# Kernel optimization log

Hardware: AMD Instinct MI355X
Metric: run time of the kernel (lower is better)

Reference implementation:

```python
import jax, jax.numpy as jnp
import numpy as np

E, N, D, H = 600000, 100000, 128, 128
LN_EPS = 1e-5


def setup_inputs() -> dict:
    key = jax.random.key(0)
    ks = jax.random.split(key, 10)
    inp = {
        "efeat": jax.random.normal(ks[0], (E, D), dtype=jnp.float32),
        "nfeat": jax.random.normal(ks[1], (N, D), dtype=jnp.float32),
        "src_idx": jax.random.randint(ks[2], (E,), 0, N, dtype=jnp.int64) if jax.config.jax_enable_x64 else jax.random.randint(ks[2], (E,), 0, N, dtype=jnp.int32),
        "dst_idx": jax.random.randint(ks[3], (E,), 0, N, dtype=jnp.int32),
        # MLP params: Linear(3D -> H) + SiLU, Linear(H -> D), LayerNorm(D)
        "W1": jax.random.normal(ks[4], (3 * D, H), dtype=jnp.float32) / np.sqrt(3 * D),
        "b1": jnp.zeros((H,), dtype=jnp.float32),
        "W2": jax.random.normal(ks[5], (H, D), dtype=jnp.float32) / np.sqrt(H),
        "b2": jnp.zeros((D,), dtype=jnp.float32),
        "ln_scale": jnp.ones((D,), dtype=jnp.float32),
        "ln_bias": jnp.zeros((D,), dtype=jnp.float32),
    }
    return inp


def _layernorm(x, scale, bias):
    mu = jnp.mean(x, axis=-1, keepdims=True)
    var = jnp.mean(jnp.square(x - mu), axis=-1, keepdims=True)
    return (x - mu) * jax.lax.rsqrt(var + LN_EPS) * scale + bias


def reference(efeat, nfeat, src_idx, dst_idx, W1, b1, W2, b2, ln_scale, ln_bias):
    # Gather per-edge source/destination node features (irregular access).
    src = nfeat[src_idx]              # [E, D]
    dst = nfeat[dst_idx]              # [E, D]
    # TMLP: equivalent to concat([efeat, src, dst]) @ W1; expressed as split GEMMs
    # so no [E, 3D] concat buffer is materialized.
    Wf, Ws, Wd = W1[:D], W1[D:2 * D], W1[2 * D:]
    h = efeat @ Wf + src @ Ws + dst @ Wd + b1   # [E, H]
    h = jax.nn.silu(h)
    y = h @ W2 + b2                              # [E, D]
    y = _layernorm(y, ln_scale, ln_bias)
    efeat_new = y + efeat                        # residual add
    return (efeat_new, nfeat)
```

## Files before the change

### kernel.cpp

```cpp
#include <hip/hip_runtime.h>
#include <stdint.h>

#define E_N 600000
#define N_N 100000

typedef short short8   __attribute__((ext_vector_type(8)));
typedef short short8a  __attribute__((ext_vector_type(8), may_alias));
typedef float floatx4  __attribute__((ext_vector_type(4)));
typedef float floatx2  __attribute__((ext_vector_type(2)));
typedef float floatx4a __attribute__((ext_vector_type(4), may_alias));
typedef float floatx8a __attribute__((ext_vector_type(8), may_alias));
typedef unsigned int uintx2  __attribute__((ext_vector_type(2)));
typedef unsigned int uintx2a __attribute__((ext_vector_type(2), may_alias));
typedef unsigned int uintx4a __attribute__((ext_vector_type(4), may_alias));
typedef __bf16 bf16x4 __attribute__((ext_vector_type(4)));
typedef __bf16 bf16x8 __attribute__((ext_vector_type(8)));

static __device__ __forceinline__ unsigned short f2bf(float f){
  unsigned u = __builtin_bit_cast(unsigned, f);
  unsigned rnd = 0x7fffu + ((u >> 16) & 1u);
  return (unsigned short)((u + rnd) >> 16);
}
static __device__ __forceinline__ unsigned pk2(float a, float b){
  floatx2 f; f[0] = a; f[1] = b;
  typedef __bf16 bf16x2 __attribute__((ext_vector_type(2)));
  return __builtin_bit_cast(unsigned, __builtin_convertvector(f, bf16x2));
}

__global__ void prep_weights(const float* __restrict__ W1, const float* __restrict__ W2,
                             unsigned short* __restrict__ w1s, unsigned short* __restrict__ w2s){
  int i = blockIdx.x * 256 + threadIdx.x;
  if (i < 384 * 128){
    int c = i / 384, k = i - c * 384;
    int p = k >> 7, kp = k & 127;
    int dw = c * 64 + ((kp >> 1) ^ ((c & 7) << 2));
    w1s[p * 16384 + dw * 2 + (k & 1)] = f2bf(W1[k * 128 + c]);
  } else {
    int j = i - 384 * 128;
    int c = j >> 7, k = j & 127;
    int dw = c * 64 + ((k >> 1) ^ ((c & 7) << 2));
    w2s[dw * 2 + (k & 1)] = f2bf(W2[k * 128 + c]);
  }
}

__global__ void prep_nfeat(const float* __restrict__ nf,
                           unsigned* __restrict__ nfbu,
                           float* __restrict__ out2){
  const int total = N_N * 128 / 4;
  int stride = gridDim.x * blockDim.x;
  for (int i = blockIdx.x * blockDim.x + threadIdx.x; i < total; i += stride){
    float4 v = reinterpret_cast<const float4*>(nf)[i];
    reinterpret_cast<float4*>(out2)[i] = v;
    nfbu[2 * i]     = pk2(v.x, v.y);
    nfbu[2 * i + 1] = pk2(v.z, v.w);
  }
}

static __device__ __forceinline__ void glds16(void* lds, const void* g){
  __builtin_amdgcn_global_load_lds((const __attribute__((address_space(1))) unsigned int*)g,
                                   (__attribute__((address_space(3))) unsigned int*)lds,
                                   16, 0, 0);
}

__global__ __launch_bounds__(512, 4) void fused_edge(
    const float* __restrict__ efeat,
    const int* __restrict__ src_idx, const int* __restrict__ dst_idx,
    const unsigned short* __restrict__ nfb,
    const unsigned short* __restrict__ w1s, const unsigned short* __restrict__ w2s,
    const float* __restrict__ b1, const float* __restrict__ b2,
    const float* __restrict__ lns, const float* __restrict__ lnb,
    float* __restrict__ out)
{
  __shared__ __align__(16) unsigned char smem[67584];
  unsigned int* wlds  = (unsigned int*)smem;
  float*        cmisc = (float*)(smem + 65536);

  const int tid  = threadIdx.x;
  const int w    = tid >> 6;
  const int lane = tid & 63;
  const int r    = lane & 15;
  const int g    = lane >> 4;
  const int sw8  = (r & 7) << 2;

  unsigned int* tile = (unsigned int*)(smem + 32768 + w * 4096);

  auto stageW = [&](const unsigned short* src){
    #pragma unroll
    for (int rnd = 0; rnd < 4; ++rnd){
      int off = rnd * 8192 + tid * 16;
      glds16(smem + off, (const unsigned char*)src + off);
    }
  };

  stageW(w1s);
  cmisc[tid] = tid < 128 ? b1[tid] : tid < 256 ? b2[tid - 128]
             : tid < 384 ? lns[tid - 256] : lnb[tid - 384];

  const int eb = blockIdx.x * 128 + w * 16;

  int e0 = eb + r;
  const int er = e0 < E_N ? e0 : (E_N - 1);
  int si = src_idx[er];
  int di = dst_idx[er];
  si = si < 0 ? 0 : (si >= N_N ? N_N - 1 : si);
  di = di < 0 ? 0 : (di >= N_N ? N_N - 1 : di);

  auto loadX_f32 = [&](const float* p) -> short8 {
    floatx8a f = *reinterpret_cast<const floatx8a*>(p);
    return __builtin_bit_cast(short8, __builtin_convertvector(f, bf16x8));
  };

  short8 xf[12];
  #pragma unroll
  for (int kf = 0; kf < 4; ++kf)
    xf[kf] = loadX_f32(efeat + (size_t)er * 128 + kf * 32 + 8 * g);
  #pragma unroll
  for (int kf = 0; kf < 4; ++kf)
    xf[4 + kf] = *reinterpret_cast<const short8a*>(nfb + (size_t)si * 128 + kf * 32 + 8 * g);
  #pragma unroll
  for (int kf = 0; kf < 4; ++kf)
    xf[8 + kf] = *reinterpret_cast<const short8a*>(nfb + (size_t)di * 128 + kf * 32 + 8 * g);

  __syncthreads();

  auto loadWL = [&](int m, int k4) -> short8 {
    uintx4a v = *reinterpret_cast<const uintx4a*>(
        &wlds[(16 * m + r) * 64 + ((k4 * 16 + 4 * g) ^ sw8)]);
    return __builtin_bit_cast(short8, v);
  };

  floatx4 acc1[8];
  #pragma unroll
  for (int mi = 0; mi < 8; ++mi)
    acc1[mi] = (floatx4){0.f, 0.f, 0.f, 0.f};

  #pragma unroll
  for (int p = 0; p < 3; ++p){
    #pragma unroll
    for (int k4 = 0; k4 < 4; ++k4){
      short8 x = xf[p * 4 + k4];
      #pragma unroll
      for (int mi = 0; mi < 8; ++mi){
        short8 wf = loadWL(mi, k4);
        acc1[mi] = __builtin_amdgcn_mfma_f32_16x16x32_bf16(wf, x, acc1[mi], 0, 0, 0);
      }
    }
    if (p == 2){
      #pragma unroll
      for (int mi = 0; mi < 8; ++mi){
        floatx4 bb = *reinterpret_cast<const floatx4a*>(&cmisc[16 * mi + 4 * g]);
        floatx4 vv;
        #pragma unroll
        for (int q = 0; q < 4; ++q){
          float xx = acc1[mi][q] + bb[q];
          vv[q] = xx * __builtin_amdgcn_rcpf(1.f + __expf(-xx));
        }
        uintx2 pk = __builtin_bit_cast(uintx2, __builtin_convertvector(vv, bf16x4));
        *reinterpret_cast<uintx2a*>(&tile[r * 64 + ((8 * mi + 2 * g) ^ sw8)]) = pk;
      }
    }
    __syncthreads();
    if (p < 2) stageW(w1s + (p + 1) * 16384);
    else       stageW(w2s);
    __syncthreads();
  }

  floatx4 acc2[8];
  #pragma unroll
  for (int mo = 0; mo < 8; ++mo)
    acc2[mo] = (floatx4){0.f, 0.f, 0.f, 0.f};

  #pragma unroll
  for (int ks = 0; ks < 4; ++ks){
    uintx4a hv = *reinterpret_cast<const uintx4a*>(&tile[r * 64 + ((ks * 16 + 4 * g) ^ sw8)]);
    short8 hb = __builtin_bit_cast(short8, hv);
    #pragma unroll
    for (int mo = 0; mo < 8; ++mo){
      short8 wf = loadWL(mo, ks);
      acc2[mo] = __builtin_amdgcn_mfma_f32_16x16x32_bf16(wf, hb, acc2[mo], 0, 0, 0);
    }
  }

  const float* ef = efeat + (size_t)er * 128;
  floatx4 e4v[8];
  #pragma unroll
  for (int mo = 0; mo < 8; ++mo)
    e4v[mo] = *reinterpret_cast<const floatx4a*>(ef + 16 * mo + 4 * g);

  float s1 = 0.f, s2 = 0.f;
  #pragma unroll
  for (int mo = 0; mo < 8; ++mo){
    floatx4 bb = *reinterpret_cast<const floatx4a*>(&cmisc[128 + 16 * mo + 4 * g]);
    #pragma unroll
    for (int q = 0; q < 4; ++q){
      float v = acc2[mo][q] + bb[q];
      s1 += v; s2 += v * v;
    }
  }
  s1 += __shfl_xor(s1, 16); s2 += __shfl_xor(s2, 16);
  s1 += __shfl_xor(s1, 32); s2 += __shfl_xor(s2, 32);

  float mu   = s1 * (1.f / 128.f);
  float var  = s2 * (1.f / 128.f) - mu * mu;
  var = var > 0.f ? var : 0.f;
  float rstd = __builtin_amdgcn_rsqf(var + 1e-5f);

  if (e0 < E_N){
    float* op = out + (size_t)e0 * 128;
    #pragma unroll
    for (int mo = 0; mo < 8; ++mo){
      int c = 16 * mo + 4 * g;
      floatx4 bb = *reinterpret_cast<const floatx4a*>(&cmisc[128 + c]);
      floatx4 ls = *reinterpret_cast<const floatx4a*>(&cmisc[256 + c]);
      floatx4 lb = *reinterpret_cast<const floatx4a*>(&cmisc[384 + c]);
      floatx4 o4;
      #pragma unroll
      for (int q = 0; q < 4; ++q)
        o4[q] = (acc2[mo][q] + bb[q] - mu) * rstd * ls[q] + lb[q] + e4v[mo][q];
      *reinterpret_cast<floatx4a*>(op + c) = o4;
    }
  }
}

extern "C" void kernel_launch(void* const* d_in, const int* in_sizes, int n_in,
                              void* d_out, int out_size, void* d_ws, size_t ws_size,
                              hipStream_t stream){
  const float* efeat = (const float*)d_in[0];
  const float* nfeat = (const float*)d_in[1];
  const int*   srci  = (const int*)d_in[2];
  const int*   dsti  = (const int*)d_in[3];
  const float* W1    = (const float*)d_in[4];
  const float* b1    = (const float*)d_in[5];
  const float* W2    = (const float*)d_in[6];
  const float* b2    = (const float*)d_in[7];
  const float* lns   = (const float*)d_in[8];
  const float* lnb   = (const float*)d_in[9];
  float* out = (float*)d_out;

  char* ws = (char*)d_ws;
  unsigned short* w1s = (unsigned short*)ws;
  unsigned short* w2s = (unsigned short*)(ws + 98304);
  unsigned short* nfb = (unsigned short*)(ws + 131072);

  prep_weights<<<(384 * 128 + 128 * 128) / 256, 256, 0, stream>>>(W1, W2, w1s, w2s);
  prep_nfeat<<<2048, 256, 0, stream>>>(nfeat, (unsigned*)nfb, out + (size_t)E_N * 128);

  int blocks = (E_N + 127) / 128;
  fused_edge<<<blocks, 512, 0, stream>>>(efeat, srci, dsti, nfb, w1s, w2s,
                                         b1, b2, lns, lnb, out);
}
```

Measured before the change: 249.2 us.

## Double-buffer weight windows in LDS and reuse bf16 efeat for residual

Weights are repacked into eight 64-row windows of 16KB, and the kernel prefetches the next window into a second LDS buffer while computing on the current one. This replaces the previous stage-then-barrier pattern, which exposed the load latency. Blocks shrink to 256 threads handling 64 edges with a smaller LDS footprint, and the edge-range bounds checks are dropped. The residual now comes from the bf16 efeat fragments already held in registers, stashed in LDS, instead of re-reading fp32 efeat from global memory. The costs are lower residual precision and twice as much weight staging per edge.

```diff
diff --git a/kernel.cpp b/kernel.cpp
--- a/kernel.cpp
+++ b/kernel.cpp
@@ -12,6 +12,7 @@
 typedef float floatx8a __attribute__((ext_vector_type(8), may_alias));
 typedef unsigned int uintx2  __attribute__((ext_vector_type(2)));
 typedef unsigned int uintx2a __attribute__((ext_vector_type(2), may_alias));
+typedef unsigned int uintx4  __attribute__((ext_vector_type(4)));
 typedef unsigned int uintx4a __attribute__((ext_vector_type(4), may_alias));
 typedef __bf16 bf16x4 __attribute__((ext_vector_type(4)));
 typedef __bf16 bf16x8 __attribute__((ext_vector_type(8)));
@@ -28,18 +29,19 @@
 }
 
 __global__ void prep_weights(const float* __restrict__ W1, const float* __restrict__ W2,
-                             unsigned short* __restrict__ w1s, unsigned short* __restrict__ w2s){
+                             unsigned short* __restrict__ wall){
   int i = blockIdx.x * 256 + threadIdx.x;
   if (i < 384 * 128){
     int c = i / 384, k = i - c * 384;
-    int p = k >> 7, kp = k & 127;
-    int dw = c * 64 + ((kp >> 1) ^ ((c & 7) << 2));
-    w1s[p * 16384 + dw * 2 + (k & 1)] = f2bf(W1[k * 128 + c]);
+    int win = k >> 6, kp = k & 63;
+    wall[win * 8192 + (c * 32 + ((kp >> 1) ^ ((c & 7) << 2))) * 2 + (kp & 1)]
+      = f2bf(W1[k * 128 + c]);
   } else {
     int j = i - 384 * 128;
     int c = j >> 7, k = j & 127;
-    int dw = c * 64 + ((k >> 1) ^ ((c & 7) << 2));
-    w2s[dw * 2 + (k & 1)] = f2bf(W2[k * 128 + c]);
+    int win = 6 + (k >> 6), kp = k & 63;
+    wall[win * 8192 + (c * 32 + ((kp >> 1) ^ ((c & 7) << 2))) * 2 + (kp & 1)]
+      = f2bf(W2[k * 128 + c]);
   }
 }
 
@@ -62,18 +64,18 @@
                                    16, 0, 0);
 }
 
-__global__ __launch_bounds__(512, 4) void fused_edge(
+__global__ __launch_bounds__(256, 3) void fused_edge(
     const float* __restrict__ efeat,
     const int* __restrict__ src_idx, const int* __restrict__ dst_idx,
     const unsigned short* __restrict__ nfb,
-    const unsigned short* __restrict__ w1s, const unsigned short* __restrict__ w2s,
+    const unsigned short* __restrict__ wall,
     const float* __restrict__ b1, const float* __restrict__ b2,
     const float* __restrict__ lns, const float* __restrict__ lnb,
     float* __restrict__ out)
 {
-  __shared__ __align__(16) unsigned char smem[67584];
-  unsigned int* wlds  = (unsigned int*)smem;
-  float*        cmisc = (float*)(smem + 65536);
+  __shared__ __align__(16) unsigned char smem[51200];
+  unsigned int* wbuf  = (unsigned int*)smem;
+  float*        cmisc = (float*)(smem + 49152);
 
   const int tid  = threadIdx.x;
   const int w    = tid >> 6;
@@ -84,24 +86,23 @@
 
   unsigned int* tile = (unsigned int*)(smem + 32768 + w * 4096);
 
-  auto stageW = [&](const unsigned short* src){
+  auto stageW = [&](int b, int win){
+    const unsigned char* src = (const unsigned char*)wall + win * 16384;
     #pragma unroll
     for (int rnd = 0; rnd < 4; ++rnd){
-      int off = rnd * 8192 + tid * 16;
-      glds16(smem + off, (const unsigned char*)src + off);
+      int off = rnd * 4096 + tid * 16;
+      glds16(smem + b * 16384 + off, src + off);
     }
   };
 
-  stageW(w1s);
-  cmisc[tid] = tid < 128 ? b1[tid] : tid < 256 ? b2[tid - 128]
-             : tid < 384 ? lns[tid - 256] : lnb[tid - 384];
-
-  const int eb = blockIdx.x * 128 + w * 16;
-
-  int e0 = eb + r;
-  const int er = e0 < E_N ? e0 : (E_N - 1);
-  int si = src_idx[er];
-  int di = dst_idx[er];
+  stageW(0, 0);
+  cmisc[tid]       = tid < 128 ? b1[tid]  : b2[tid - 128];
+  cmisc[tid + 256] = tid < 128 ? lns[tid] : lnb[tid - 128];
+
+  const int eb = blockIdx.x * 64 + w * 16;
+  const int e0 = eb + r;
+  int si = src_idx[e0];
+  int di = dst_idx[e0];
   si = si < 0 ? 0 : (si >= N_N ? N_N - 1 : si);
   di = di < 0 ? 0 : (di >= N_N ? N_N - 1 : di);
 
@@ -113,7 +114,7 @@
   short8 xf[12];
   #pragma unroll
   for (int kf = 0; kf < 4; ++kf)
-    xf[kf] = loadX_f32(efeat + (size_t)er * 128 + kf * 32 + 8 * g);
+    xf[kf] = loadX_f32(efeat + (size_t)e0 * 128 + kf * 32 + 8 * g);
   #pragma unroll
   for (int kf = 0; kf < 4; ++kf)
     xf[4 + kf] = *reinterpret_cast<const short8a*>(nfb + (size_t)si * 128 + kf * 32 + 8 * g);
@@ -123,9 +124,9 @@
 
   __syncthreads();
 
-  auto loadWL = [&](int m, int k4) -> short8 {
+  auto loadWL = [&](int b, int m, int k2) -> short8 {
     uintx4a v = *reinterpret_cast<const uintx4a*>(
-        &wlds[(16 * m + r) * 64 + ((k4 * 16 + 4 * g) ^ sw8)]);
+        &wbuf[b * 4096 + (16 * m + r) * 32 + ((k2 * 16 + 4 * g) ^ sw8)]);
     return __builtin_bit_cast(short8, v);
   };
 
@@ -135,17 +136,19 @@
     acc1[mi] = (floatx4){0.f, 0.f, 0.f, 0.f};
 
   #pragma unroll
-  for (int p = 0; p < 3; ++p){
-    #pragma unroll
-    for (int k4 = 0; k4 < 4; ++k4){
-      short8 x = xf[p * 4 + k4];
+  for (int t = 0; t < 6; ++t){
+    stageW((t + 1) & 1, t + 1);
+    const int b = t & 1;
+    #pragma unroll
+    for (int k2 = 0; k2 < 2; ++k2){
+      short8 x = xf[2 * t + k2];
       #pragma unroll
       for (int mi = 0; mi < 8; ++mi){
-        short8 wf = loadWL(mi, k4);
+        short8 wf = loadWL(b, mi, k2);
         acc1[mi] = __builtin_amdgcn_mfma_f32_16x16x32_bf16(wf, x, acc1[mi], 0, 0, 0);
       }
     }
-    if (p == 2){
+    if (t == 5){
       #pragma unroll
       for (int mi = 0; mi < 8; ++mi){
         floatx4 bb = *reinterpret_cast<const floatx4a*>(&cmisc[16 * mi + 4 * g]);
@@ -160,9 +163,6 @@
       }
     }
     __syncthreads();
-    if (p < 2) stageW(w1s + (p + 1) * 16384);
-    else       stageW(w2s);
-    __syncthreads();
   }
 
   floatx4 acc2[8];
@@ -171,21 +171,27 @@
     acc2[mo] = (floatx4){0.f, 0.f, 0.f, 0.f};
 
   #pragma unroll
-  for (int ks = 0; ks < 4; ++ks){
-    uintx4a hv = *reinterpret_cast<const uintx4a*>(&tile[r * 64 + ((ks * 16 + 4 * g) ^ sw8)]);
-    short8 hb = __builtin_bit_cast(short8, hv);
-    #pragma unroll
-    for (int mo = 0; mo < 8; ++mo){
-      short8 wf = loadWL(mo, ks);
-      acc2[mo] = __builtin_amdgcn_mfma_f32_16x16x32_bf16(wf, hb, acc2[mo], 0, 0, 0);
-    }
-  }
-
-  const float* ef = efeat + (size_t)er * 128;
-  floatx4 e4v[8];
-  #pragma unroll
-  for (int mo = 0; mo < 8; ++mo)
-    e4v[mo] = *reinterpret_cast<const floatx4a*>(ef + 16 * mo + 4 * g);
+  for (int t = 6; t < 8; ++t){
+    if (t < 7) stageW((t + 1) & 1, t + 1);
+    const int b = t & 1;
+    #pragma unroll
+    for (int k2 = 0; k2 < 2; ++k2){
+      const int ks = 2 * (t - 6) + k2;
+      uintx4a hv = *reinterpret_cast<const uintx4a*>(&tile[r * 64 + ((ks * 16 + 4 * g) ^ sw8)]);
+      short8 hb = __builtin_bit_cast(short8, hv);
+      #pragma unroll
+      for (int mo = 0; mo < 8; ++mo){
+        short8 wf = loadWL(b, mo, k2);
+        acc2[mo] = __builtin_amdgcn_mfma_f32_16x16x32_bf16(wf, hb, acc2[mo], 0, 0, 0);
+      }
+    }
+    if (t < 7) __syncthreads();
+  }
+
+  #pragma unroll
+  for (int kf = 0; kf < 4; ++kf)
+    *reinterpret_cast<uintx4a*>(&tile[r * 64 + ((16 * kf + 4 * g) ^ sw8)]) =
+        __builtin_bit_cast(uintx4, xf[kf]);
 
   float s1 = 0.f, s2 = 0.f;
   #pragma unroll
@@ -205,20 +211,24 @@
   var = var > 0.f ? var : 0.f;
   float rstd = __builtin_amdgcn_rsqf(var + 1e-5f);
 
-  if (e0 < E_N){
-    float* op = out + (size_t)e0 * 128;
-    #pragma unroll
-    for (int mo = 0; mo < 8; ++mo){
-      int c = 16 * mo + 4 * g;
-      floatx4 bb = *reinterpret_cast<const floatx4a*>(&cmisc[128 + c]);
-      floatx4 ls = *reinterpret_cast<const floatx4a*>(&cmisc[256 + c]);
-      floatx4 lb = *reinterpret_cast<const floatx4a*>(&cmisc[384 + c]);
-      floatx4 o4;
-      #pragma unroll
-      for (int q = 0; q < 4; ++q)
-        o4[q] = (acc2[mo][q] + bb[q] - mu) * rstd * ls[q] + lb[q] + e4v[mo][q];
-      *reinterpret_cast<floatx4a*>(op + c) = o4;
-    }
+  float* op = out + (size_t)e0 * 128;
+  #pragma unroll
+  for (int mo = 0; mo < 8; ++mo){
+    int c = 16 * mo + 4 * g;
+    floatx4 bb = *reinterpret_cast<const floatx4a*>(&cmisc[128 + c]);
+    floatx4 ls = *reinterpret_cast<const floatx4a*>(&cmisc[256 + c]);
+    floatx4 lb = *reinterpret_cast<const floatx4a*>(&cmisc[384 + c]);
+    uintx2a rv = *reinterpret_cast<const uintx2a*>(&tile[r * 64 + ((8 * mo + 2 * g) ^ sw8)]);
+    floatx4 e4;
+    e4[0] = __builtin_bit_cast(float, rv[0] << 16);
+    e4[1] = __builtin_bit_cast(float, rv[0] & 0xffff0000u);
+    e4[2] = __builtin_bit_cast(float, rv[1] << 16);
+    e4[3] = __builtin_bit_cast(float, rv[1] & 0xffff0000u);
+    floatx4 o4;
+    #pragma unroll
+    for (int q = 0; q < 4; ++q)
+      o4[q] = (acc2[mo][q] + bb[q] - mu) * rstd * ls[q] + lb[q] + e4[q];
+    *reinterpret_cast<floatx4a*>(op + c) = o4;
   }
 }
 
@@ -238,14 +248,13 @@
   float* out = (float*)d_out;
 
   char* ws = (char*)d_ws;
-  unsigned short* w1s = (unsigned short*)ws;
-  unsigned short* w2s = (unsigned short*)(ws + 98304);
-  unsigned short* nfb = (unsigned short*)(ws + 131072);
-
-  prep_weights<<<(384 * 128 + 128 * 128) / 256, 256, 0, stream>>>(W1, W2, w1s, w2s);
+  unsigned short* wall = (unsigned short*)ws;
+  unsigned short* nfb  = (unsigned short*)(ws + 131072);
+
+  prep_weights<<<(384 * 128 + 128 * 128) / 256, 256, 0, stream>>>(W1, W2, wall);
   prep_nfeat<<<2048, 256, 0, stream>>>(nfeat, (unsigned*)nfb, out + (size_t)E_N * 128);
 
-  int blocks = (E_N + 127) / 128;
-  fused_edge<<<blocks, 512, 0, stream>>>(efeat, srci, dsti, nfb, w1s, w2s,
+  int blocks = E_N / 64;
+  fused_edge<<<blocks, 256, 0, stream>>>(efeat, srci, dsti, nfb, wall,
                                          b1, b2, lns, lnb, out);
 }
```

Result: faster. 234.2 us (-6.0%).
